# Kernel optimization log

Hardware: AMD Instinct MI355X
Metric: run time of the kernel (lower is better)

Reference implementation:

```python
import jax, jax.numpy as jnp
import numpy as np

B, C, HEADS, W, Hh = 8, 512, 8, 32, 32
D = C // HEADS  # 64 per-head dim
N = W * Hh      # 1024 spatial tokens


def setup_inputs() -> dict:
    key = jax.random.key(0)
    ks = jax.random.split(key, 10)
    s = 1.0 / np.sqrt(C)
    return {
        "x": jax.random.normal(ks[0], (B, C, W, Hh), dtype=jnp.float32),
        "Wq": jax.random.normal(ks[1], (C, C), dtype=jnp.float32) * s,
        "bq": jax.random.normal(ks[2], (C,), dtype=jnp.float32) * 0.01,
        "Wk": jax.random.normal(ks[3], (C, C), dtype=jnp.float32) * s,
        "bk": jax.random.normal(ks[4], (C,), dtype=jnp.float32) * 0.01,
        "Wv": jax.random.normal(ks[5], (C, C), dtype=jnp.float32) * s,
        "bv": jax.random.normal(ks[6], (C,), dtype=jnp.float32) * 0.01,
        "rel_h": jax.random.normal(ks[7], (1, HEADS, D, 1, Hh), dtype=jnp.float32),
        "rel_w": jax.random.normal(ks[8], (1, HEADS, D, W, 1), dtype=jnp.float32),
    }


def reference(x, Wq, bq, Wk, bk, Wv, bv, rel_h, rel_w):
    b = x.shape[0]
    xf = x.reshape(b, C, N)  # [B, C, N] — 1x1 conv == per-position linear
    proj = lambda Wm, bm: (jnp.einsum('oc,bcn->bon', Wm, xf) + bm[None, :, None]).reshape(b, HEADS, D, N)
    q = proj(Wq, bq)  # [B, H, D, N]
    k = proj(Wk, bk)
    v = proj(Wv, bv)
    # content-content: q^T k -> [B, H, N, N]
    cc = jnp.einsum('bhdn,bhdm->bhnm', q, k)
    # relative position bias: (rel_h + rel_w) -> [H, D, N], then rel^T @ q
    rel = (rel_h + rel_w).reshape(HEADS, D, N)
    cp = jnp.einsum('hdn,bhdm->bhnm', rel, q)  # [B, H, N, N]
    attn = jax.nn.softmax(cc + cp, axis=-1)
    # out = v @ attn^T : out[d,m] = sum_n v[d,n] * attn[m,n]
    out = jnp.einsum('bhdn,bhmn->bhdm', v, attn)  # [B, H, D, N]
    return out.reshape(b, C, W, Hh)
```

## Files before the change

kernel.cpp:

```cpp
#include <hip/hip_runtime.h>

typedef short short8 __attribute__((ext_vector_type(8)));
typedef _Float16 half8 __attribute__((ext_vector_type(8)));
typedef _Float16 half4 __attribute__((ext_vector_type(4)));
typedef float f32x4 __attribute__((ext_vector_type(4)));

__device__ __forceinline__ void glds16(const void* g, void* l) {
    __builtin_amdgcn_global_load_lds(
        (const __attribute__((address_space(1))) unsigned int*)g,
        (__attribute__((address_space(3))) unsigned int*)l, 16, 0, 0);
}


__global__ void k_pack_w(const float* __restrict__ Wq, const float* __restrict__ Wk,
                         const float* __restrict__ Wv, const float* __restrict__ bq,
                         const float* __restrict__ bk, const float* __restrict__ bv,
                         _Float16* __restrict__ Wf, float* __restrict__ bias2) {
    int t = blockIdx.x * 256 + threadIdx.x;
    int m = t >> 6;
    int c8 = (t & 63) << 3;
    const float* src = (m < 512) ? (Wq + m * 512)
                     : (m < 1024 ? (Wk + (m - 512) * 512) : (Wv + (m - 1024) * 512));
    float4 v0 = *(const float4*)(src + c8);
    float4 v1 = *(const float4*)(src + c8 + 4);
    half8 o;
    o[0] = (_Float16)v0.x; o[1] = (_Float16)v0.y; o[2] = (_Float16)v0.z; o[3] = (_Float16)v0.w;
    o[4] = (_Float16)v1.x; o[5] = (_Float16)v1.y; o[6] = (_Float16)v1.z; o[7] = (_Float16)v1.w;
    *(half8*)(Wf + (size_t)m * 512 + c8) = o;
    if (t < 1536)
        bias2[t] = (t < 512) ? bq[t] : (t < 1024 ? bk[t - 512] : bv[t - 1024]);
}

__global__ void k_prep_x(const float* __restrict__ x, _Float16* __restrict__ xTf) {
    __shared__ float xs[64][65];
    int nt = blockIdx.x * 64, ct = blockIdx.y * 64, b = blockIdx.z;
    int t = threadIdx.x;
    const float* xb = x + ((size_t)b * 512 + ct) * 1024 + nt;
#pragma unroll
    for (int p = 0; p < 4; ++p) {
        int c = p * 16 + (t >> 4), n4 = (t & 15) * 4;
        float4 v = *(const float4*)(xb + (size_t)c * 1024 + n4);
        xs[c][n4] = v.x; xs[c][n4 + 1] = v.y; xs[c][n4 + 2] = v.z; xs[c][n4 + 3] = v.w;
    }
    __syncthreads();
    int nl = t >> 2, part = t & 3;
    _Float16* rowp = xTf + ((size_t)b * 1024 + nt + nl) * 512;
#pragma unroll
    for (int g = 0; g < 2; ++g) {
        half8 o;
#pragma unroll
        for (int j = 0; j < 8; ++j)
            o[j] = (_Float16)xs[part * 16 + g * 8 + j][nl];
        *(half8*)(rowp + ct + part * 16 + g * 8) = o;
    }
}

__global__ void k_prep_rel(const float* __restrict__ rel_h, const float* __restrict__ rel_w,
                           _Float16* __restrict__ rel2) {
    int tid = blockIdx.x * 256 + threadIdx.x;
    int h = tid >> 13;
    int rem = tid & 8191;
    int n = rem >> 3;
    int g = rem & 7;
    int hh = n & 31, ww = n >> 5;
    half8 o;
#pragma unroll
    for (int j = 0; j < 8; ++j) {
        int d = g * 8 + j;
        o[j] = (_Float16)(rel_h[(h * 64 + d) * 32 + hh] + rel_w[(h * 64 + d) * 32 + ww]);
    }
    *(half8*)(rel2 + ((size_t)h * 1024 + n) * 64 + g * 8) = o;
}

__global__ __launch_bounds__(256, 3) void k_proj(const _Float16* __restrict__ Wf,
                                                 const _Float16* __restrict__ xTf,
                                                 const float* __restrict__ bias2,
                                                 _Float16* __restrict__ q2,
                                                 _Float16* __restrict__ k2,
                                                 _Float16* __restrict__ vb) {
    __shared__ __align__(16) _Float16 As[8192];
    __shared__ __align__(16) _Float16 Bs[8192];
    int t = threadIdx.x;
    int lane = t & 63, w = t >> 6;
    int lm = lane & 15, lq = lane >> 4;
    int wr = (w >> 1) * 64, wc = (w & 1) * 64;
    int mb = blockIdx.y * 128, nb = blockIdx.x * 128, b = blockIdx.z;
    int rl = lane >> 2;
    int csw = ((lane & 3) ^ ((lane >> 3) & 3)) * 8;
    const _Float16* Ag0 = Wf + (size_t)(mb + w * 32 + rl) * 512 + csw;
    const _Float16* Ag1 = Ag0 + 16 * 512;
    const _Float16* Bg0 = xTf + ((size_t)b * 1024 + nb + w * 32 + rl) * 512 + csw;
    const _Float16* Bg1 = Bg0 + 16 * 512;
    f32x4 acc[4][4];
#pragma unroll
    for (int i = 0; i < 4; ++i)
#pragma unroll
        for (int j = 0; j < 4; ++j) acc[i][j] = {0.f, 0.f, 0.f, 0.f};
    int fsw = (lq ^ ((lm >> 1) & 3)) * 8;
    for (int k0 = 0; k0 < 512; k0 += 64) {
#pragma unroll
        for (int kh = 0; kh < 2; ++kh) {
            int ko = k0 + kh * 32;
            glds16(Ag0 + ko, &As[kh * 4096 + (w * 32) * 32]);
            glds16(Ag1 + ko, &As[kh * 4096 + (w * 32 + 16) * 32]);
            glds16(Bg0 + ko, &Bs[kh * 4096 + (w * 32) * 32]);
            glds16(Bg1 + ko, &Bs[kh * 4096 + (w * 32 + 16) * 32]);
        }
        __syncthreads();
#pragma unroll
        for (int kh = 0; kh < 2; ++kh) {
            half8 af[4], bfr[4];
#pragma unroll
            for (int mt = 0; mt < 4; ++mt)
                af[mt] = *(half8*)&As[kh * 4096 + (wr + mt * 16 + lm) * 32 + fsw];
#pragma unroll
            for (int nt = 0; nt < 4; ++nt)
                bfr[nt] = *(half8*)&Bs[kh * 4096 + (wc + nt * 16 + lm) * 32 + fsw];
#pragma unroll
            for (int mt = 0; mt < 4; ++mt)
#pragma unroll
                for (int nt = 0; nt < 4; ++nt)
                    acc[mt][nt] = __builtin_amdgcn_mfma_f32_16x16x32_f16(af[mt], bfr[nt], acc[mt][nt], 0, 0, 0);
        }
        __syncthreads();
    }
    int sect = mb >> 9;
    int hloc = ((mb & 511) + wr) >> 6;
    size_t bh = (size_t)b * 8 + hloc;
    if (sect < 2) {
        _Float16* dst = (sect == 0 ? q2 : k2) + bh * 1024 * 64;
#pragma unroll
        for (int mt = 0; mt < 4; ++mt) {
            int d0 = mt * 16 + lq * 4;
            float bi0 = bias2[mb + wr + d0];
            float bi1 = bias2[mb + wr + d0 + 1];
            float bi2 = bias2[mb + wr + d0 + 2];
            float bi3 = bias2[mb + wr + d0 + 3];
#pragma unroll
            for (int nt = 0; nt < 4; ++nt) {
                int n = nb + wc + nt * 16 + lm;
                half4 o;
                o[0] = (_Float16)(acc[mt][nt][0] + bi0);
                o[1] = (_Float16)(acc[mt][nt][1] + bi1);
                o[2] = (_Float16)(acc[mt][nt][2] + bi2);
                o[3] = (_Float16)(acc[mt][nt][3] + bi3);
                *(half4*)(dst + (size_t)n * 64 + d0) = o;
            }
        }
    } else {
        _Float16* dst = vb + bh * 64 * 1024;
#pragma unroll
        for (int mt = 0; mt < 4; ++mt)
#pragma unroll
            for (int reg = 0; reg < 4; ++reg) {
                int d = mt * 16 + lq * 4 + reg;
                float bi = bias2[mb + wr + d];
#pragma unroll
                for (int nt = 0; nt < 4; ++nt) {
                    int n = nb + wc + nt * 16 + lm;
                    dst[(size_t)d * 1024 + n] = (_Float16)(acc[mt][nt][reg] + bi);
                }
            }
    }
}

__global__ __launch_bounds__(256, 4) void k_attn(const _Float16* __restrict__ q2,
                                                 const _Float16* __restrict__ k2,
                                                 const _Float16* __restrict__ rel2,
                                                 const _Float16* __restrict__ vb,
                                                 float* __restrict__ out) {
    __shared__ __align__(16) char pool[35840];
    _Float16* kb_s = (_Float16*)pool;
    _Float16* v_s  = (_Float16*)(pool + 17408);
    _Float16* p_s  = (_Float16*)(pool + 26624);
    int t = threadIdx.x;
    int lane = t & 63, w = t >> 6;
    int lm = lane & 15, lq = lane >> 4;
    int lin = blockIdx.x;
    int mt0 = lin >> 6;
    int bh_ = lin & 63;
    int h = bh_ & 7, b = bh_ >> 3;
    size_t bh = (size_t)b * 8 + h;
    const _Float16* q2b = q2 + bh * 1024 * 64;
    const _Float16* k2b = k2 + bh * 1024 * 64;
    const _Float16* relb = rel2 + (size_t)h * 1024 * 64;
    const _Float16* vbb = vb + bh * 64 * 1024;
    float* outb = out + bh * 64 * 1024 + mt0 * 64;

    int r = t >> 2, part = t & 3;
    const _Float16* ksrc = ((part < 2) ? (k2b + part * 32) : (q2b + (part - 2) * 32));
    int vc = (t & 3) * 16;
    const _Float16* vsrcb = vbb + (size_t)r * 1024 + vc;
    _Float16* kdst = kb_s + r * 136 + part * 32;
    _Float16* vdst = v_s + r * 72 + vc;

    uint4 kc0, kc1, kc2, kc3, vv0, vv1;
    {
        const uint4* s_ = (const uint4*)(ksrc + (size_t)r * 64);
        kc0 = s_[0]; kc1 = s_[1]; kc2 = s_[2]; kc3 = s_[3];
        const uint4* v_ = (const uint4*)vsrcb;
        vv0 = v_[0]; vv1 = v_[1];
    }

    {
        int n = mt0 * 64 + r;
        const _Float16* src = (part < 2) ? (q2b + (size_t)n * 64 + part * 32)
                                         : (relb + (size_t)n * 64 + (part - 2) * 32);
        ((uint4*)kdst)[0] = ((const uint4*)src)[0];
        ((uint4*)kdst)[1] = ((const uint4*)src)[1];
        ((uint4*)kdst)[2] = ((const uint4*)src)[2];
        ((uint4*)kdst)[3] = ((const uint4*)src)[3];
    }
    __syncthreads();
    half8 ah[4];
#pragma unroll
    for (int kk = 0; kk < 4; ++kk)
        ah[kk] = *(half8*)&kb_s[(w * 16 + lm) * 136 + kk * 32 + lq * 8];
    f32x4 acco[4];
#pragma unroll
    for (int i = 0; i < 4; ++i) acco[i] = {0.f, 0.f, 0.f, 0.f};
    float mrun = -3e38f, lrun = 0.f;

    for (int kt = 0; kt < 16; ++kt) {
        ((uint4*)kdst)[0] = kc0;
        ((uint4*)kdst)[1] = kc1;
        ((uint4*)kdst)[2] = kc2;
        ((uint4*)kdst)[3] = kc3;
        ((uint4*)vdst)[0] = vv0;
        ((uint4*)vdst)[1] = vv1;
        __syncthreads();
        int nn = ((kt + 1) & 15) * 64;
        const uint4* s_ = (const uint4*)(ksrc + (size_t)(nn + r) * 64);
        uint4 kn0 = s_[0], kn1 = s_[1], kn2 = s_[2], kn3 = s_[3];
        const uint4* v_ = (const uint4*)(vsrcb + nn);
        uint4 vn0 = v_[0], vn1 = v_[1];
        f32x4 sac[4];
#pragma unroll
        for (int ct = 0; ct < 4; ++ct) sac[ct] = {0.f, 0.f, 0.f, 0.f};
#pragma unroll
        for (int ct = 0; ct < 4; ++ct) {
            half8 kf[4];
#pragma unroll
            for (int kk = 0; kk < 4; ++kk)
                kf[kk] = *(half8*)&kb_s[(ct * 16 + lm) * 136 + kk * 32 + lq * 8];
#pragma unroll
            for (int kk = 0; kk < 4; ++kk)
                sac[ct] = __builtin_amdgcn_mfma_f32_16x16x32_f16(kf[kk], ah[kk], sac[ct], 0, 0, 0);
        }
        float mx = -3e38f;
#pragma unroll
        for (int ct = 0; ct < 4; ++ct)
#pragma unroll
            for (int reg = 0; reg < 4; ++reg) mx = fmaxf(mx, sac[ct][reg]);
        mx = fmaxf(mx, __shfl_xor(mx, 16));
        mx = fmaxf(mx, __shfl_xor(mx, 32));
        float mnew = fmaxf(mrun, mx);
        float al_ = __expf(mrun - mnew);
        float ps[4][4];
        float rs = 0.f;
#pragma unroll
        for (int ct = 0; ct < 4; ++ct)
#pragma unroll
            for (int reg = 0; reg < 4; ++reg) {
                float p = __expf(sac[ct][reg] - mnew);
                ps[ct][reg] = p;
                rs += p;
            }
        rs += __shfl_xor(rs, 16);
        rs += __shfl_xor(rs, 32);
        lrun = lrun * al_ + rs;
        mrun = mnew;
#pragma unroll
        for (int dt = 0; dt < 4; ++dt) {
            acco[dt][0] *= al_; acco[dt][1] *= al_;
            acco[dt][2] *= al_; acco[dt][3] *= al_;
        }
#pragma unroll
        for (int ct = 0; ct < 4; ++ct) {
            half4 o;
            o[0] = (_Float16)ps[ct][0]; o[1] = (_Float16)ps[ct][1];
            o[2] = (_Float16)ps[ct][2]; o[3] = (_Float16)ps[ct][3];
            *(half4*)&p_s[(w * 16 + lm) * 72 + ct * 16 + lq * 4] = o;
        }
        half8 pfr[2];
#pragma unroll
        for (int ch = 0; ch < 2; ++ch)
            pfr[ch] = *(half8*)&p_s[(w * 16 + lm) * 72 + ch * 32 + lq * 8];
#pragma unroll
        for (int dt = 0; dt < 4; ++dt) {
            half8 vf0 = *(half8*)&v_s[(dt * 16 + lm) * 72 + lq * 8];
            half8 vf1 = *(half8*)&v_s[(dt * 16 + lm) * 72 + 32 + lq * 8];
            acco[dt] = __builtin_amdgcn_mfma_f32_16x16x32_f16(vf0, pfr[0], acco[dt], 0, 0, 0);
            acco[dt] = __builtin_amdgcn_mfma_f32_16x16x32_f16(vf1, pfr[1], acco[dt], 0, 0, 0);
        }
        __syncthreads();
        kc0 = kn0; kc1 = kn1; kc2 = kn2; kc3 = kn3;
        vv0 = vn0; vv1 = vn1;
    }
    float li = 1.f / lrun;
#pragma unroll
    for (int dt = 0; dt < 4; ++dt)
#pragma unroll
        for (int reg = 0; reg < 4; ++reg) {
            int d = dt * 16 + lq * 4 + reg;
            outb[(size_t)d * 1024 + w * 16 + lm] = acco[dt][reg] * li;
        }
}

extern "C" void kernel_launch(void* const* d_in, const int* in_sizes, int n_in,
                              void* d_out, int out_size, void* d_ws, size_t ws_size,
                              hipStream_t stream) {
    const float* x     = (const float*)d_in[0];
    const float* Wq    = (const float*)d_in[1];
    const float* bq    = (const float*)d_in[2];
    const float* Wk    = (const float*)d_in[3];
    const float* bk    = (const float*)d_in[4];
    const float* Wv    = (const float*)d_in[5];
    const float* bv    = (const float*)d_in[6];
    const float* rel_h = (const float*)d_in[7];
    const float* rel_w = (const float*)d_in[8];
    char* ws = (char*)d_ws;
    _Float16* Wf   = (_Float16*)(ws);
    float* bias2   = (float*)(ws + 1572864);
    _Float16* xTf  = (_Float16*)(ws + 1579008);
    _Float16* q2   = (_Float16*)(ws + 9967616);
    _Float16* k2   = (_Float16*)(ws + 18356224);
    _Float16* vb   = (_Float16*)(ws + 26744832);
    _Float16* rel2 = (_Float16*)(ws + 35133440);
    float* out = (float*)d_out;

    hipLaunchKernelGGL(k_pack_w,   dim3(384),      dim3(256), 0, stream, Wq, Wk, Wv, bq, bk, bv, Wf, bias2);
    hipLaunchKernelGGL(k_prep_x,   dim3(16, 8, 8), dim3(256), 0, stream, x, xTf);
    hipLaunchKernelGGL(k_prep_rel, dim3(256),      dim3(256), 0, stream, rel_h, rel_w, rel2);
    hipLaunchKernelGGL(k_proj,     dim3(8, 12, 8), dim3(256), 0, stream, Wf, xTf, bias2, q2, k2, vb);
    hipLaunchKernelGGL(k_attn,     dim3(1024),     dim3(256), 0, stream, q2, k2, rel2, vb, out);
}
```

Measured before the change: 161.2 us.

## Process two query tiles per attention block, fold log2e into Q, merge prep kernels

Each attention block now handles 128 query rows as two 64-row sub-tiles that share every K/V tile staged in LDS, which halves the grid and the K/V reload traffic. The projection epilogue pre-scales Q by log2(e), so the softmax can use exp2f instead of __expf. Because both the content and positional score terms are linear in q, this scaling stays correct. The three preprocessing kernels are merged into one launch with block-index dispatch. In exchange the block uses more registers and LDS (occupancy hint lowered from 4 to 3) and runs fewer blocks, which may underfill the GPU.

Result: faster. 153.0 us (-5.1%).

```diff
diff --git a/kernel.cpp b/kernel.cpp
--- a/kernel.cpp
+++ b/kernel.cpp
@@ -1,6 +1,5 @@
 #include <hip/hip_runtime.h>
 
-typedef short short8 __attribute__((ext_vector_type(8)));
 typedef _Float16 half8 __attribute__((ext_vector_type(8)));
 typedef _Float16 half4 __attribute__((ext_vector_type(4)));
 typedef float f32x4 __attribute__((ext_vector_type(4)));
@@ -12,64 +11,66 @@
 }
 
 
-__global__ void k_pack_w(const float* __restrict__ Wq, const float* __restrict__ Wk,
-                         const float* __restrict__ Wv, const float* __restrict__ bq,
-                         const float* __restrict__ bk, const float* __restrict__ bv,
-                         _Float16* __restrict__ Wf, float* __restrict__ bias2) {
-    int t = blockIdx.x * 256 + threadIdx.x;
-    int m = t >> 6;
-    int c8 = (t & 63) << 3;
-    const float* src = (m < 512) ? (Wq + m * 512)
-                     : (m < 1024 ? (Wk + (m - 512) * 512) : (Wv + (m - 1024) * 512));
-    float4 v0 = *(const float4*)(src + c8);
-    float4 v1 = *(const float4*)(src + c8 + 4);
-    half8 o;
-    o[0] = (_Float16)v0.x; o[1] = (_Float16)v0.y; o[2] = (_Float16)v0.z; o[3] = (_Float16)v0.w;
-    o[4] = (_Float16)v1.x; o[5] = (_Float16)v1.y; o[6] = (_Float16)v1.z; o[7] = (_Float16)v1.w;
-    *(half8*)(Wf + (size_t)m * 512 + c8) = o;
-    if (t < 1536)
-        bias2[t] = (t < 512) ? bq[t] : (t < 1024 ? bk[t - 512] : bv[t - 1024]);
-}
-
-__global__ void k_prep_x(const float* __restrict__ x, _Float16* __restrict__ xTf) {
+__global__ void k_prep_all(const float* __restrict__ Wq, const float* __restrict__ Wk,
+                           const float* __restrict__ Wv, const float* __restrict__ bq,
+                           const float* __restrict__ bk, const float* __restrict__ bv,
+                           const float* __restrict__ x, const float* __restrict__ rel_h,
+                           const float* __restrict__ rel_w, _Float16* __restrict__ Wf,
+                           float* __restrict__ bias2, _Float16* __restrict__ xTf,
+                           _Float16* __restrict__ rel2) {
     __shared__ float xs[64][65];
-    int nt = blockIdx.x * 64, ct = blockIdx.y * 64, b = blockIdx.z;
-    int t = threadIdx.x;
-    const float* xb = x + ((size_t)b * 512 + ct) * 1024 + nt;
-#pragma unroll
-    for (int p = 0; p < 4; ++p) {
-        int c = p * 16 + (t >> 4), n4 = (t & 15) * 4;
-        float4 v = *(const float4*)(xb + (size_t)c * 1024 + n4);
-        xs[c][n4] = v.x; xs[c][n4 + 1] = v.y; xs[c][n4 + 2] = v.z; xs[c][n4 + 3] = v.w;
-    }
-    __syncthreads();
-    int nl = t >> 2, part = t & 3;
-    _Float16* rowp = xTf + ((size_t)b * 1024 + nt + nl) * 512;
-#pragma unroll
-    for (int g = 0; g < 2; ++g) {
+    int bid = blockIdx.x;
+    if (bid < 384) {
+        int t = bid * 256 + threadIdx.x;
+        int m = t >> 6;
+        int c8 = (t & 63) << 3;
+        const float* src = (m < 512) ? (Wq + m * 512)
+                         : (m < 1024 ? (Wk + (m - 512) * 512) : (Wv + (m - 1024) * 512));
+        float4 v0 = *(const float4*)(src + c8);
+        float4 v1 = *(const float4*)(src + c8 + 4);
         half8 o;
-#pragma unroll
-        for (int j = 0; j < 8; ++j)
-            o[j] = (_Float16)xs[part * 16 + g * 8 + j][nl];
-        *(half8*)(rowp + ct + part * 16 + g * 8) = o;
-    }
-}
-
-__global__ void k_prep_rel(const float* __restrict__ rel_h, const float* __restrict__ rel_w,
-                           _Float16* __restrict__ rel2) {
-    int tid = blockIdx.x * 256 + threadIdx.x;
-    int h = tid >> 13;
-    int rem = tid & 8191;
-    int n = rem >> 3;
-    int g = rem & 7;
-    int hh = n & 31, ww = n >> 5;
-    half8 o;
-#pragma unroll
-    for (int j = 0; j < 8; ++j) {
-        int d = g * 8 + j;
-        o[j] = (_Float16)(rel_h[(h * 64 + d) * 32 + hh] + rel_w[(h * 64 + d) * 32 + ww]);
-    }
-    *(half8*)(rel2 + ((size_t)h * 1024 + n) * 64 + g * 8) = o;
+        o[0] = (_Float16)v0.x; o[1] = (_Float16)v0.y; o[2] = (_Float16)v0.z; o[3] = (_Float16)v0.w;
+        o[4] = (_Float16)v1.x; o[5] = (_Float16)v1.y; o[6] = (_Float16)v1.z; o[7] = (_Float16)v1.w;
+        *(half8*)(Wf + (size_t)m * 512 + c8) = o;
+        if (t < 1536)
+            bias2[t] = (t < 512) ? bq[t] : (t < 1024 ? bk[t - 512] : bv[t - 1024]);
+    } else if (bid < 1408) {
+        int i = bid - 384;
+        int nt = (i & 15) << 6, ct = ((i >> 4) & 7) << 6, b = i >> 7;
+        int t = threadIdx.x;
+        const float* xb = x + ((size_t)b * 512 + ct) * 1024 + nt;
+#pragma unroll
+        for (int p = 0; p < 4; ++p) {
+            int c = p * 16 + (t >> 4), n4 = (t & 15) * 4;
+            float4 v = *(const float4*)(xb + (size_t)c * 1024 + n4);
+            xs[c][n4] = v.x; xs[c][n4 + 1] = v.y; xs[c][n4 + 2] = v.z; xs[c][n4 + 3] = v.w;
+        }
+        __syncthreads();
+        int nl = t >> 2, part = t & 3;
+        _Float16* rowp = xTf + ((size_t)b * 1024 + nt + nl) * 512;
+#pragma unroll
+        for (int g = 0; g < 2; ++g) {
+            half8 o;
+#pragma unroll
+            for (int j = 0; j < 8; ++j)
+                o[j] = (_Float16)xs[part * 16 + g * 8 + j][nl];
+            *(half8*)(rowp + ct + part * 16 + g * 8) = o;
+        }
+    } else {
+        int tid = (bid - 1408) * 256 + threadIdx.x;
+        int h = tid >> 13;
+        int rem = tid & 8191;
+        int n = rem >> 3;
+        int g = rem & 7;
+        int hh = n & 31, ww = n >> 5;
+        half8 o;
+#pragma unroll
+        for (int j = 0; j < 8; ++j) {
+            int d = g * 8 + j;
+            o[j] = (_Float16)(rel_h[(h * 64 + d) * 32 + hh] + rel_w[(h * 64 + d) * 32 + ww]);
+        }
+        *(half8*)(rel2 + ((size_t)h * 1024 + n) * 64 + g * 8) = o;
+    }
 }
 
 __global__ __launch_bounds__(256, 3) void k_proj(const _Float16* __restrict__ Wf,
@@ -128,6 +129,7 @@
     int hloc = ((mb & 511) + wr) >> 6;
     size_t bh = (size_t)b * 8 + hloc;
     if (sect < 2) {
+        float sc = (sect == 0) ? 1.44269504089f : 1.0f;
         _Float16* dst = (sect == 0 ? q2 : k2) + bh * 1024 * 64;
 #pragma unroll
         for (int mt = 0; mt < 4; ++mt) {
@@ -140,10 +142,10 @@
             for (int nt = 0; nt < 4; ++nt) {
                 int n = nb + wc + nt * 16 + lm;
                 half4 o;
-                o[0] = (_Float16)(acc[mt][nt][0] + bi0);
-                o[1] = (_Float16)(acc[mt][nt][1] + bi1);
-                o[2] = (_Float16)(acc[mt][nt][2] + bi2);
-                o[3] = (_Float16)(acc[mt][nt][3] + bi3);
+                o[0] = (_Float16)((acc[mt][nt][0] + bi0) * sc);
+                o[1] = (_Float16)((acc[mt][nt][1] + bi1) * sc);
+                o[2] = (_Float16)((acc[mt][nt][2] + bi2) * sc);
+                o[3] = (_Float16)((acc[mt][nt][3] + bi3) * sc);
                 *(half4*)(dst + (size_t)n * 64 + d0) = o;
             }
         }
@@ -164,12 +166,12 @@
     }
 }
 
-__global__ __launch_bounds__(256, 4) void k_attn(const _Float16* __restrict__ q2,
+__global__ __launch_bounds__(256, 3) void k_attn(const _Float16* __restrict__ q2,
                                                  const _Float16* __restrict__ k2,
                                                  const _Float16* __restrict__ rel2,
                                                  const _Float16* __restrict__ vb,
                                                  float* __restrict__ out) {
-    __shared__ __align__(16) char pool[35840];
+    __shared__ __align__(16) char pool[45056];
     _Float16* kb_s = (_Float16*)pool;
     _Float16* v_s  = (_Float16*)(pool + 17408);
     _Float16* p_s  = (_Float16*)(pool + 26624);
@@ -185,7 +187,7 @@
     const _Float16* k2b = k2 + bh * 1024 * 64;
     const _Float16* relb = rel2 + (size_t)h * 1024 * 64;
     const _Float16* vbb = vb + bh * 64 * 1024;
-    float* outb = out + bh * 64 * 1024 + mt0 * 64;
+    float* outb = out + bh * 64 * 1024 + mt0 * 128;
 
     int r = t >> 2, part = t & 3;
     const _Float16* ksrc = ((part < 2) ? (k2b + part * 32) : (q2b + (part - 2) * 32));
@@ -203,7 +205,7 @@
     }
 
     {
-        int n = mt0 * 64 + r;
+        int n = mt0 * 128 + r;
         const _Float16* src = (part < 2) ? (q2b + (size_t)n * 64 + part * 32)
                                          : (relb + (size_t)n * 64 + (part - 2) * 32);
         ((uint4*)kdst)[0] = ((const uint4*)src)[0];
@@ -212,14 +214,30 @@
         ((uint4*)kdst)[3] = ((const uint4*)src)[3];
     }
     __syncthreads();
-    half8 ah[4];
+    half8 ah0[4], ah1[4];
 #pragma unroll
     for (int kk = 0; kk < 4; ++kk)
-        ah[kk] = *(half8*)&kb_s[(w * 16 + lm) * 136 + kk * 32 + lq * 8];
-    f32x4 acco[4];
-#pragma unroll
-    for (int i = 0; i < 4; ++i) acco[i] = {0.f, 0.f, 0.f, 0.f};
-    float mrun = -3e38f, lrun = 0.f;
+        ah0[kk] = *(half8*)&kb_s[(w * 16 + lm) * 136 + kk * 32 + lq * 8];
+    __syncthreads();
+    {
+        int n = mt0 * 128 + 64 + r;
+        const _Float16* src = (part < 2) ? (q2b + (size_t)n * 64 + part * 32)
+                                         : (relb + (size_t)n * 64 + (part - 2) * 32);
+        ((uint4*)kdst)[0] = ((const uint4*)src)[0];
+        ((uint4*)kdst)[1] = ((const uint4*)src)[1];
+        ((uint4*)kdst)[2] = ((const uint4*)src)[2];
+        ((uint4*)kdst)[3] = ((const uint4*)src)[3];
+    }
+    __syncthreads();
+#pragma unroll
+    for (int kk = 0; kk < 4; ++kk)
+        ah1[kk] = *(half8*)&kb_s[(w * 16 + lm) * 136 + kk * 32 + lq * 8];
+    __syncthreads();
+
+    f32x4 acco0[4], acco1[4];
+#pragma unroll
+    for (int i = 0; i < 4; ++i) { acco0[i] = {0.f, 0.f, 0.f, 0.f}; acco1[i] = {0.f, 0.f, 0.f, 0.f}; }
+    float mrun0 = -3e38f, lrun0 = 0.f, mrun1 = -3e38f, lrun1 = 0.f;
 
     for (int kt = 0; kt < 16; ++kt) {
         ((uint4*)kdst)[0] = kc0;
@@ -234,9 +252,9 @@
         uint4 kn0 = s_[0], kn1 = s_[1], kn2 = s_[2], kn3 = s_[3];
         const uint4* v_ = (const uint4*)(vsrcb + nn);
         uint4 vn0 = v_[0], vn1 = v_[1];
-        f32x4 sac[4];
-#pragma unroll
-        for (int ct = 0; ct < 4; ++ct) sac[ct] = {0.f, 0.f, 0.f, 0.f};
+        f32x4 s0[4], s1[4];
+#pragma unroll
+        for (int ct = 0; ct < 4; ++ct) { s0[ct] = {0.f, 0.f, 0.f, 0.f}; s1[ct] = {0.f, 0.f, 0.f, 0.f}; }
 #pragma unroll
         for (int ct = 0; ct < 4; ++ct) {
             half8 kf[4];
@@ -244,66 +262,100 @@
             for (int kk = 0; kk < 4; ++kk)
                 kf[kk] = *(half8*)&kb_s[(ct * 16 + lm) * 136 + kk * 32 + lq * 8];
 #pragma unroll
-            for (int kk = 0; kk < 4; ++kk)
-                sac[ct] = __builtin_amdgcn_mfma_f32_16x16x32_f16(kf[kk], ah[kk], sac[ct], 0, 0, 0);
-        }
-        float mx = -3e38f;
-#pragma unroll
-        for (int ct = 0; ct < 4; ++ct)
-#pragma unroll
-            for (int reg = 0; reg < 4; ++reg) mx = fmaxf(mx, sac[ct][reg]);
-        mx = fmaxf(mx, __shfl_xor(mx, 16));
-        mx = fmaxf(mx, __shfl_xor(mx, 32));
-        float mnew = fmaxf(mrun, mx);
-        float al_ = __expf(mrun - mnew);
-        float ps[4][4];
-        float rs = 0.f;
-#pragma unroll
-        for (int ct = 0; ct < 4; ++ct)
-#pragma unroll
-            for (int reg = 0; reg < 4; ++reg) {
-                float p = __expf(sac[ct][reg] - mnew);
-                ps[ct][reg] = p;
-                rs += p;
-            }
-        rs += __shfl_xor(rs, 16);
-        rs += __shfl_xor(rs, 32);
-        lrun = lrun * al_ + rs;
-        mrun = mnew;
-#pragma unroll
-        for (int dt = 0; dt < 4; ++dt) {
-            acco[dt][0] *= al_; acco[dt][1] *= al_;
-            acco[dt][2] *= al_; acco[dt][3] *= al_;
-        }
-#pragma unroll
-        for (int ct = 0; ct < 4; ++ct) {
-            half4 o;
-            o[0] = (_Float16)ps[ct][0]; o[1] = (_Float16)ps[ct][1];
-            o[2] = (_Float16)ps[ct][2]; o[3] = (_Float16)ps[ct][3];
-            *(half4*)&p_s[(w * 16 + lm) * 72 + ct * 16 + lq * 4] = o;
-        }
-        half8 pfr[2];
-#pragma unroll
-        for (int ch = 0; ch < 2; ++ch)
-            pfr[ch] = *(half8*)&p_s[(w * 16 + lm) * 72 + ch * 32 + lq * 8];
+            for (int kk = 0; kk < 4; ++kk) {
+                s0[ct] = __builtin_amdgcn_mfma_f32_16x16x32_f16(kf[kk], ah0[kk], s0[ct], 0, 0, 0);
+                s1[ct] = __builtin_amdgcn_mfma_f32_16x16x32_f16(kf[kk], ah1[kk], s1[ct], 0, 0, 0);
+            }
+        }
+        {
+            float mx = -3e38f;
+#pragma unroll
+            for (int ct = 0; ct < 4; ++ct)
+#pragma unroll
+                for (int reg = 0; reg < 4; ++reg) mx = fmaxf(mx, s0[ct][reg]);
+            mx = fmaxf(mx, __shfl_xor(mx, 16));
+            mx = fmaxf(mx, __shfl_xor(mx, 32));
+            float mnew = fmaxf(mrun0, mx);
+            float al_ = exp2f(mrun0 - mnew);
+            float rs = 0.f;
+#pragma unroll
+            for (int ct = 0; ct < 4; ++ct) {
+                float p0 = exp2f(s0[ct][0] - mnew);
+                float p1 = exp2f(s0[ct][1] - mnew);
+                float p2 = exp2f(s0[ct][2] - mnew);
+                float p3 = exp2f(s0[ct][3] - mnew);
+                rs += (p0 + p1) + (p2 + p3);
+                half4 o; o[0] = (_Float16)p0; o[1] = (_Float16)p1; o[2] = (_Float16)p2; o[3] = (_Float16)p3;
+                *(half4*)&p_s[(w * 16 + lm) * 72 + ct * 16 + lq * 4] = o;
+            }
+            rs += __shfl_xor(rs, 16);
+            rs += __shfl_xor(rs, 32);
+            lrun0 = lrun0 * al_ + rs;
+            mrun0 = mnew;
+#pragma unroll
+            for (int dt = 0; dt < 4; ++dt) {
+                acco0[dt][0] *= al_; acco0[dt][1] *= al_;
+                acco0[dt][2] *= al_; acco0[dt][3] *= al_;
+            }
+        }
+        {
+            float mx = -3e38f;
+#pragma unroll
+            for (int ct = 0; ct < 4; ++ct)
+#pragma unroll
+                for (int reg = 0; reg < 4; ++reg) mx = fmaxf(mx, s1[ct][reg]);
+            mx = fmaxf(mx, __shfl_xor(mx, 16));
+            mx = fmaxf(mx, __shfl_xor(mx, 32));
+            float mnew = fmaxf(mrun1, mx);
+            float al_ = exp2f(mrun1 - mnew);
+            float rs = 0.f;
+#pragma unroll
+            for (int ct = 0; ct < 4; ++ct) {
+                float p0 = exp2f(s1[ct][0] - mnew);
+                float p1 = exp2f(s1[ct][1] - mnew);
+                float p2 = exp2f(s1[ct][2] - mnew);
+                float p3 = exp2f(s1[ct][3] - mnew);
+                rs += (p0 + p1) + (p2 + p3);
+                half4 o; o[0] = (_Float16)p0; o[1] = (_Float16)p1; o[2] = (_Float16)p2; o[3] = (_Float16)p3;
+                *(half4*)&p_s[(64 + w * 16 + lm) * 72 + ct * 16 + lq * 4] = o;
+            }
+            rs += __shfl_xor(rs, 16);
+            rs += __shfl_xor(rs, 32);
+            lrun1 = lrun1 * al_ + rs;
+            mrun1 = mnew;
+#pragma unroll
+            for (int dt = 0; dt < 4; ++dt) {
+                acco1[dt][0] *= al_; acco1[dt][1] *= al_;
+                acco1[dt][2] *= al_; acco1[dt][3] *= al_;
+            }
+        }
+        half8 p0f[2], p1f[2];
+#pragma unroll
+        for (int ch = 0; ch < 2; ++ch) {
+            p0f[ch] = *(half8*)&p_s[(w * 16 + lm) * 72 + ch * 32 + lq * 8];
+            p1f[ch] = *(half8*)&p_s[(64 + w * 16 + lm) * 72 + ch * 32 + lq * 8];
+        }
 #pragma unroll
         for (int dt = 0; dt < 4; ++dt) {
             half8 vf0 = *(half8*)&v_s[(dt * 16 + lm) * 72 + lq * 8];
             half8 vf1 = *(half8*)&v_s[(dt * 16 + lm) * 72 + 32 + lq * 8];
-            acco[dt] = __builtin_amdgcn_mfma_f32_16x16x32_f16(vf0, pfr[0], acco[dt], 0, 0, 0);
-            acco[dt] = __builtin_amdgcn_mfma_f32_16x16x32_f16(vf1, pfr[1], acco[dt], 0, 0, 0);
+            acco0[dt] = __builtin_amdgcn_mfma_f32_16x16x32_f16(vf0, p0f[0], acco0[dt], 0, 0, 0);
+            acco0[dt] = __builtin_amdgcn_mfma_f32_16x16x32_f16(vf1, p0f[1], acco0[dt], 0, 0, 0);
+            acco1[dt] = __builtin_amdgcn_mfma_f32_16x16x32_f16(vf0, p1f[0], acco1[dt], 0, 0, 0);
+            acco1[dt] = __builtin_amdgcn_mfma_f32_16x16x32_f16(vf1, p1f[1], acco1[dt], 0, 0, 0);
         }
         __syncthreads();
         kc0 = kn0; kc1 = kn1; kc2 = kn2; kc3 = kn3;
         vv0 = vn0; vv1 = vn1;
     }
-    float li = 1.f / lrun;
+    float li0 = 1.f / lrun0, li1 = 1.f / lrun1;
 #pragma unroll
     for (int dt = 0; dt < 4; ++dt)
 #pragma unroll
         for (int reg = 0; reg < 4; ++reg) {
             int d = dt * 16 + lq * 4 + reg;
-            outb[(size_t)d * 1024 + w * 16 + lm] = acco[dt][reg] * li;
+            outb[(size_t)d * 1024 + w * 16 + lm] = acco0[dt][reg] * li0;
+            outb[(size_t)d * 1024 + 64 + w * 16 + lm] = acco1[dt][reg] * li1;
         }
 }
 
@@ -329,9 +381,8 @@
     _Float16* rel2 = (_Float16*)(ws + 35133440);
     float* out = (float*)d_out;
 
-    hipLaunchKernelGGL(k_pack_w,   dim3(384),      dim3(256), 0, stream, Wq, Wk, Wv, bq, bk, bv, Wf, bias2);
-    hipLaunchKernelGGL(k_prep_x,   dim3(16, 8, 8), dim3(256), 0, stream, x, xTf);
-    hipLaunchKernelGGL(k_prep_rel, dim3(256),      dim3(256), 0, stream, rel_h, rel_w, rel2);
+    hipLaunchKernelGGL(k_prep_all, dim3(1664),     dim3(256), 0, stream,
+                       Wq, Wk, Wv, bq, bk, bv, x, rel_h, rel_w, Wf, bias2, xTf, rel2);
     hipLaunchKernelGGL(k_proj,     dim3(8, 12, 8), dim3(256), 0, stream, Wf, xTf, bias2, q2, k2, vb);
-    hipLaunchKernelGGL(k_attn,     dim3(1024),     dim3(256), 0, stream, q2, k2, rel2, vb, out);
-}
+    hipLaunchKernelGGL(k_attn,     dim3(512),      dim3(256), 0, stream, q2, k2, rel2, vb, out);
+}
```

## Stage projection epilogue through LDS, merge prep kernels, use exp2 softmax

Applied to the files above, without the earlier changes.

The projection epilogue now writes the biased tile into shared memory, then emits coalesced 16-byte stores for Q/K and a transposed, vectorised store for V. This replaces the scattered 2-byte V stores and the strided Q/K stores. The three preprocessing kernels are merged into one launch with block-range dispatch, removing two launch gaps. Q is pre-scaled by log2(e) so the online softmax can use exp2f directly, and the P store is folded into the exponent loop. The cost is an extra LDS round trip and barrier in the projection epilogue, plus a larger shared allocation there.

Measured after the change: 160.6 us. About the same (-0.3%).

```diff
diff --git a/kernel.cpp b/kernel.cpp
--- a/kernel.cpp
+++ b/kernel.cpp
@@ -1,6 +1,5 @@
 #include <hip/hip_runtime.h>
 
-typedef short short8 __attribute__((ext_vector_type(8)));
 typedef _Float16 half8 __attribute__((ext_vector_type(8)));
 typedef _Float16 half4 __attribute__((ext_vector_type(4)));
 typedef float f32x4 __attribute__((ext_vector_type(4)));
@@ -12,64 +11,66 @@
 }
 
 
-__global__ void k_pack_w(const float* __restrict__ Wq, const float* __restrict__ Wk,
-                         const float* __restrict__ Wv, const float* __restrict__ bq,
-                         const float* __restrict__ bk, const float* __restrict__ bv,
-                         _Float16* __restrict__ Wf, float* __restrict__ bias2) {
-    int t = blockIdx.x * 256 + threadIdx.x;
-    int m = t >> 6;
-    int c8 = (t & 63) << 3;
-    const float* src = (m < 512) ? (Wq + m * 512)
-                     : (m < 1024 ? (Wk + (m - 512) * 512) : (Wv + (m - 1024) * 512));
-    float4 v0 = *(const float4*)(src + c8);
-    float4 v1 = *(const float4*)(src + c8 + 4);
-    half8 o;
-    o[0] = (_Float16)v0.x; o[1] = (_Float16)v0.y; o[2] = (_Float16)v0.z; o[3] = (_Float16)v0.w;
-    o[4] = (_Float16)v1.x; o[5] = (_Float16)v1.y; o[6] = (_Float16)v1.z; o[7] = (_Float16)v1.w;
-    *(half8*)(Wf + (size_t)m * 512 + c8) = o;
-    if (t < 1536)
-        bias2[t] = (t < 512) ? bq[t] : (t < 1024 ? bk[t - 512] : bv[t - 1024]);
-}
-
-__global__ void k_prep_x(const float* __restrict__ x, _Float16* __restrict__ xTf) {
+__global__ void k_prep_all(const float* __restrict__ Wq, const float* __restrict__ Wk,
+                           const float* __restrict__ Wv, const float* __restrict__ bq,
+                           const float* __restrict__ bk, const float* __restrict__ bv,
+                           const float* __restrict__ x, const float* __restrict__ rel_h,
+                           const float* __restrict__ rel_w, _Float16* __restrict__ Wf,
+                           float* __restrict__ bias2, _Float16* __restrict__ xTf,
+                           _Float16* __restrict__ rel2) {
     __shared__ float xs[64][65];
-    int nt = blockIdx.x * 64, ct = blockIdx.y * 64, b = blockIdx.z;
-    int t = threadIdx.x;
-    const float* xb = x + ((size_t)b * 512 + ct) * 1024 + nt;
-#pragma unroll
-    for (int p = 0; p < 4; ++p) {
-        int c = p * 16 + (t >> 4), n4 = (t & 15) * 4;
-        float4 v = *(const float4*)(xb + (size_t)c * 1024 + n4);
-        xs[c][n4] = v.x; xs[c][n4 + 1] = v.y; xs[c][n4 + 2] = v.z; xs[c][n4 + 3] = v.w;
-    }
-    __syncthreads();
-    int nl = t >> 2, part = t & 3;
-    _Float16* rowp = xTf + ((size_t)b * 1024 + nt + nl) * 512;
-#pragma unroll
-    for (int g = 0; g < 2; ++g) {
+    int bid = blockIdx.x;
+    if (bid < 384) {
+        int t = bid * 256 + threadIdx.x;
+        int m = t >> 6;
+        int c8 = (t & 63) << 3;
+        const float* src = (m < 512) ? (Wq + m * 512)
+                         : (m < 1024 ? (Wk + (m - 512) * 512) : (Wv + (m - 1024) * 512));
+        float4 v0 = *(const float4*)(src + c8);
+        float4 v1 = *(const float4*)(src + c8 + 4);
         half8 o;
-#pragma unroll
-        for (int j = 0; j < 8; ++j)
-            o[j] = (_Float16)xs[part * 16 + g * 8 + j][nl];
-        *(half8*)(rowp + ct + part * 16 + g * 8) = o;
-    }
-}
-
-__global__ void k_prep_rel(const float* __restrict__ rel_h, const float* __restrict__ rel_w,
-                           _Float16* __restrict__ rel2) {
-    int tid = blockIdx.x * 256 + threadIdx.x;
-    int h = tid >> 13;
-    int rem = tid & 8191;
-    int n = rem >> 3;
-    int g = rem & 7;
-    int hh = n & 31, ww = n >> 5;
-    half8 o;
-#pragma unroll
-    for (int j = 0; j < 8; ++j) {
-        int d = g * 8 + j;
-        o[j] = (_Float16)(rel_h[(h * 64 + d) * 32 + hh] + rel_w[(h * 64 + d) * 32 + ww]);
-    }
-    *(half8*)(rel2 + ((size_t)h * 1024 + n) * 64 + g * 8) = o;
+        o[0] = (_Float16)v0.x; o[1] = (_Float16)v0.y; o[2] = (_Float16)v0.z; o[3] = (_Float16)v0.w;
+        o[4] = (_Float16)v1.x; o[5] = (_Float16)v1.y; o[6] = (_Float16)v1.z; o[7] = (_Float16)v1.w;
+        *(half8*)(Wf + (size_t)m * 512 + c8) = o;
+        if (t < 1536)
+            bias2[t] = (t < 512) ? bq[t] : (t < 1024 ? bk[t - 512] : bv[t - 1024]);
+    } else if (bid < 1408) {
+        int i = bid - 384;
+        int nt = (i & 15) << 6, ct = ((i >> 4) & 7) << 6, b = i >> 7;
+        int t = threadIdx.x;
+        const float* xb = x + ((size_t)b * 512 + ct) * 1024 + nt;
+#pragma unroll
+        for (int p = 0; p < 4; ++p) {
+            int c = p * 16 + (t >> 4), n4 = (t & 15) * 4;
+            float4 v = *(const float4*)(xb + (size_t)c * 1024 + n4);
+            xs[c][n4] = v.x; xs[c][n4 + 1] = v.y; xs[c][n4 + 2] = v.z; xs[c][n4 + 3] = v.w;
+        }
+        __syncthreads();
+        int nl = t >> 2, part = t & 3;
+        _Float16* rowp = xTf + ((size_t)b * 1024 + nt + nl) * 512;
+#pragma unroll
+        for (int g = 0; g < 2; ++g) {
+            half8 o;
+#pragma unroll
+            for (int j = 0; j < 8; ++j)
+                o[j] = (_Float16)xs[part * 16 + g * 8 + j][nl];
+            *(half8*)(rowp + ct + part * 16 + g * 8) = o;
+        }
+    } else {
+        int tid = (bid - 1408) * 256 + threadIdx.x;
+        int h = tid >> 13;
+        int rem = tid & 8191;
+        int n = rem >> 3;
+        int g = rem & 7;
+        int hh = n & 31, ww = n >> 5;
+        half8 o;
+#pragma unroll
+        for (int j = 0; j < 8; ++j) {
+            int d = g * 8 + j;
+            o[j] = (_Float16)(rel_h[(h * 64 + d) * 32 + hh] + rel_w[(h * 64 + d) * 32 + ww]);
+        }
+        *(half8*)(rel2 + ((size_t)h * 1024 + n) * 64 + g * 8) = o;
+    }
 }
 
 __global__ __launch_bounds__(256, 3) void k_proj(const _Float16* __restrict__ Wf,
@@ -78,8 +79,10 @@
                                                  _Float16* __restrict__ q2,
                                                  _Float16* __restrict__ k2,
                                                  _Float16* __restrict__ vb) {
-    __shared__ __align__(16) _Float16 As[8192];
-    __shared__ __align__(16) _Float16 Bs[8192];
+    __shared__ __align__(16) char pool[34816];
+    _Float16* As = (_Float16*)pool;
+    _Float16* Bs = (_Float16*)(pool + 16384);
+    _Float16* ts = (_Float16*)pool;
     int t = threadIdx.x;
     int lane = t & 63, w = t >> 6;
     int lm = lane & 15, lq = lane >> 4;
@@ -125,42 +128,56 @@
         __syncthreads();
     }
     int sect = mb >> 9;
-    int hloc = ((mb & 511) + wr) >> 6;
-    size_t bh = (size_t)b * 8 + hloc;
+    int h0 = (mb & 511) >> 6;
+    float sc = (sect == 0) ? 1.44269504089f : 1.0f;
+#pragma unroll
+    for (int mt = 0; mt < 4; ++mt) {
+        int d0 = wr + mt * 16 + lq * 4;
+        float bi0 = bias2[mb + d0];
+        float bi1 = bias2[mb + d0 + 1];
+        float bi2 = bias2[mb + d0 + 2];
+        float bi3 = bias2[mb + d0 + 3];
+#pragma unroll
+        for (int nt = 0; nt < 4; ++nt) {
+            int n = wc + nt * 16 + lm;
+            half4 o;
+            o[0] = (_Float16)((acc[mt][nt][0] + bi0) * sc);
+            o[1] = (_Float16)((acc[mt][nt][1] + bi1) * sc);
+            o[2] = (_Float16)((acc[mt][nt][2] + bi2) * sc);
+            o[3] = (_Float16)((acc[mt][nt][3] + bi3) * sc);
+            *(half4*)&ts[n * 136 + d0] = o;
+        }
+    }
+    __syncthreads();
     if (sect < 2) {
-        _Float16* dst = (sect == 0 ? q2 : k2) + bh * 1024 * 64;
-#pragma unroll
-        for (int mt = 0; mt < 4; ++mt) {
-            int d0 = mt * 16 + lq * 4;
-            float bi0 = bias2[mb + wr + d0];
-            float bi1 = bias2[mb + wr + d0 + 1];
-            float bi2 = bias2[mb + wr + d0 + 2];
-            float bi3 = bias2[mb + wr + d0 + 3];
-#pragma unroll
-            for (int nt = 0; nt < 4; ++nt) {
-                int n = nb + wc + nt * 16 + lm;
-                half4 o;
-                o[0] = (_Float16)(acc[mt][nt][0] + bi0);
-                o[1] = (_Float16)(acc[mt][nt][1] + bi1);
-                o[2] = (_Float16)(acc[mt][nt][2] + bi2);
-                o[3] = (_Float16)(acc[mt][nt][3] + bi3);
-                *(half4*)(dst + (size_t)n * 64 + d0) = o;
+        _Float16* base = (sect == 0 ? q2 : k2);
+#pragma unroll
+        for (int hh = 0; hh < 2; ++hh) {
+            size_t bh = (size_t)b * 8 + h0 + hh;
+            _Float16* dst = base + (bh * 1024 + nb) * 64;
+#pragma unroll
+            for (int i = 0; i < 4; ++i) {
+                int u = i * 256 + t;
+                int n = u >> 3, c = u & 7;
+                *(uint4*)(dst + (size_t)n * 64 + c * 8) = *(uint4*)&ts[n * 136 + hh * 64 + c * 8];
             }
         }
     } else {
-        _Float16* dst = vb + bh * 64 * 1024;
-#pragma unroll
-        for (int mt = 0; mt < 4; ++mt)
-#pragma unroll
-            for (int reg = 0; reg < 4; ++reg) {
-                int d = mt * 16 + lq * 4 + reg;
-                float bi = bias2[mb + wr + d];
-#pragma unroll
-                for (int nt = 0; nt < 4; ++nt) {
-                    int n = nb + wc + nt * 16 + lm;
-                    dst[(size_t)d * 1024 + n] = (_Float16)(acc[mt][nt][reg] + bi);
-                }
+#pragma unroll
+        for (int hh = 0; hh < 2; ++hh) {
+            size_t bh = (size_t)b * 8 + h0 + hh;
+            _Float16* dst = vb + bh * 64 * 1024 + nb;
+#pragma unroll
+            for (int i = 0; i < 4; ++i) {
+                int u = i * 256 + t;
+                int d = u >> 4, c = u & 15;
+                half8 o;
+#pragma unroll
+                for (int j = 0; j < 8; ++j)
+                    o[j] = ts[(c * 8 + j) * 136 + hh * 64 + d];
+                *(half8*)(dst + (size_t)d * 1024 + c * 8) = o;
             }
+        }
     }
 }
 
@@ -255,17 +272,18 @@
         mx = fmaxf(mx, __shfl_xor(mx, 16));
         mx = fmaxf(mx, __shfl_xor(mx, 32));
         float mnew = fmaxf(mrun, mx);
-        float al_ = __expf(mrun - mnew);
-        float ps[4][4];
+        float al_ = exp2f(mrun - mnew);
         float rs = 0.f;
 #pragma unroll
-        for (int ct = 0; ct < 4; ++ct)
-#pragma unroll
-            for (int reg = 0; reg < 4; ++reg) {
-                float p = __expf(sac[ct][reg] - mnew);
-                ps[ct][reg] = p;
-                rs += p;
-            }
+        for (int ct = 0; ct < 4; ++ct) {
+            float p0 = exp2f(sac[ct][0] - mnew);
+            float p1 = exp2f(sac[ct][1] - mnew);
+            float p2 = exp2f(sac[ct][2] - mnew);
+            float p3 = exp2f(sac[ct][3] - mnew);
+            rs += (p0 + p1) + (p2 + p3);
+            half4 o; o[0] = (_Float16)p0; o[1] = (_Float16)p1; o[2] = (_Float16)p2; o[3] = (_Float16)p3;
+            *(half4*)&p_s[(w * 16 + lm) * 72 + ct * 16 + lq * 4] = o;
+        }
         rs += __shfl_xor(rs, 16);
         rs += __shfl_xor(rs, 32);
         lrun = lrun * al_ + rs;
@@ -274,13 +292,6 @@
         for (int dt = 0; dt < 4; ++dt) {
             acco[dt][0] *= al_; acco[dt][1] *= al_;
             acco[dt][2] *= al_; acco[dt][3] *= al_;
-        }
-#pragma unroll
-        for (int ct = 0; ct < 4; ++ct) {
-            half4 o;
-            o[0] = (_Float16)ps[ct][0]; o[1] = (_Float16)ps[ct][1];
-            o[2] = (_Float16)ps[ct][2]; o[3] = (_Float16)ps[ct][3];
-            *(half4*)&p_s[(w * 16 + lm) * 72 + ct * 16 + lq * 4] = o;
         }
         half8 pfr[2];
 #pragma unroll
@@ -329,9 +340,8 @@
     _Float16* rel2 = (_Float16*)(ws + 35133440);
     float* out = (float*)d_out;
 
-    hipLaunchKernelGGL(k_pack_w,   dim3(384),      dim3(256), 0, stream, Wq, Wk, Wv, bq, bk, bv, Wf, bias2);
-    hipLaunchKernelGGL(k_prep_x,   dim3(16, 8, 8), dim3(256), 0, stream, x, xTf);
-    hipLaunchKernelGGL(k_prep_rel, dim3(256),      dim3(256), 0, stream, rel_h, rel_w, rel2);
+    hipLaunchKernelGGL(k_prep_all, dim3(1664),     dim3(256), 0, stream,
+                       Wq, Wk, Wv, bq, bk, bv, x, rel_h, rel_w, Wf, bias2, xTf, rel2);
     hipLaunchKernelGGL(k_proj,     dim3(8, 12, 8), dim3(256), 0, stream, Wf, xTf, bias2, q2, k2, vb);
     hipLaunchKernelGGL(k_attn,     dim3(1024),     dim3(256), 0, stream, q2, k2, rel2, vb, out);
 }
```
